# Kernel optimization log

Hardware: AMD Instinct MI355X
Metric: run time of the kernel (lower is better)

Reference implementation:

```python
import jax, jax.numpy as jnp
import numpy as np

B, T = 64, 256
CHAR_V, CHAR_D = 8000, 128
WORD_V, WORD_D = 100000, 300
POS_V, POS_D = 30, 64
SPO_D = 20
D = CHAR_D + WORD_D + POS_D + SPO_D  # 512
L, H, KD, VD, INNER = 4, 8, 64, 64, 2048
C = 25  # num tag classes


def _layer_norm(x, g, b, eps=1e-5):
    m = jnp.mean(x, axis=-1, keepdims=True)
    v = jnp.mean(jnp.square(x - m), axis=-1, keepdims=True)
    return (x - m) * jax.lax.rsqrt(v + eps) * g + b


def setup_inputs() -> dict:
    key = jax.random.key(0)
    ks = jax.random.split(key, 40)
    s = 0.05
    n = lambda k, shp, sc=0.05: jax.random.normal(k, shp, jnp.float32) * sc
    return {
        "char": jax.random.randint(ks[0], (B, T), 0, CHAR_V),
        "word": jax.random.randint(ks[1], (B, T), 0, WORD_V),
        "pos": jax.random.randint(ks[2], (B, T), 0, POS_V),
        "spo": jax.random.normal(ks[3], (B, SPO_D), jnp.float32),
        "seq_len": jax.random.randint(ks[4], (B,), 1, T + 1),
        "tag": jax.random.randint(ks[5], (B, T), 0, C),
        "char_table": n(ks[6], (CHAR_V, CHAR_D)),
        "word_table": n(ks[7], (WORD_V, WORD_D)),
        "pos_table": n(ks[8], (POS_V, POS_D)),
        "ln0_g": jnp.ones((D,), jnp.float32),
        "ln0_b": jnp.zeros((D,), jnp.float32),
        "Wq": n(ks[9], (L, D, H * KD)), "bq": jnp.zeros((L, H * KD), jnp.float32),
        "Wk": n(ks[10], (L, D, H * KD)), "bk": jnp.zeros((L, H * KD), jnp.float32),
        "Wv": n(ks[11], (L, D, H * VD)), "bv": jnp.zeros((L, H * VD), jnp.float32),
        "Wo": n(ks[12], (L, H * VD, D)), "bo": jnp.zeros((L, D), jnp.float32),
        "ln1_g": jnp.ones((L, D), jnp.float32), "ln1_b": jnp.zeros((L, D), jnp.float32),
        "W1": n(ks[13], (L, D, INNER)), "b1": jnp.zeros((L, INNER), jnp.float32),
        "W2": n(ks[14], (L, INNER, D)), "b2": jnp.zeros((L, D), jnp.float32),
        "ln2_g": jnp.ones((L, D), jnp.float32), "ln2_b": jnp.zeros((L, D), jnp.float32),
        "Wout": n(ks[15], (D, C)), "bout": jnp.zeros((C,), jnp.float32),
        "trans": n(ks[16], (C, C)),
    }


def _forward(spo, char_table, word_table, pos_table, ln0_g, ln0_b,
             Wq, bq, Wk, bk, Wv, bv, Wo, bo, ln1_g, ln1_b,
             W1, b1, W2, b2, ln2_g, ln2_b, Wout, bout, trans,
             char, word, pos, seq_len, tag):
    # mask[b,t] = t < seq_len[b]
    mask = (jnp.arange(T)[None, :] < seq_len[:, None]).astype(jnp.float32)  # [B,T]

    # embed + concat + layernorm (dropout in eval mode = identity)
    x = jnp.concatenate([
        char_table[char], word_table[word], pos_table[pos],
        jnp.broadcast_to(spo[:, None, :], (B, T, SPO_D)),
    ], axis=-1)  # [B,T,D]
    x = _layer_norm(x, ln0_g, ln0_b)

    neg_inf = jnp.finfo(x.dtype).min
    key_ok = mask[:, None, None, :] > 0  # [B,1,1,T] key padding mask
    scale = jnp.sqrt(jnp.asarray(KD, x.dtype))
    for l in range(L):
        q = (x @ Wq[l] + bq[l]).reshape(B, T, H, KD).transpose(0, 2, 1, 3)
        k = (x @ Wk[l] + bk[l]).reshape(B, T, H, KD).transpose(0, 2, 1, 3)
        v = (x @ Wv[l] + bv[l]).reshape(B, T, H, VD).transpose(0, 2, 1, 3)
        scores = jnp.einsum('bhqd,bhkd->bhqk', q, k) / scale
        scores = jnp.where(key_ok, scores, neg_inf)
        attn = jax.nn.softmax(scores, axis=-1)
        ctx = jnp.einsum('bhqk,bhkd->bhqd', attn, v).transpose(0, 2, 1, 3).reshape(B, T, H * VD)
        att_out = ctx @ Wo[l] + bo[l]
        h1 = _layer_norm(att_out + x, ln1_g[l], ln1_b[l])
        ff = jax.nn.relu(h1 @ W1[l] + b1[l]) @ W2[l] + b2[l]
        x = _layer_norm(ff + h1, ln2_g[l], ln2_b[l]) * mask[:, :, None]

    logits = x @ Wout + bout  # [B,T,C]

    # ---- CRF negative log likelihood (include_start_end_trans=False) ----
    lg = logits.transpose(1, 0, 2)  # [T,B,C]
    m = mask.T                      # [T,B]

    def step(alpha, inp):
        emit, mt = inp  # emit [B,C], mt [B]
        tmp = alpha[:, :, None] + trans[None, :, :] + emit[:, None, :]  # [B,C,C]
        new = jax.nn.logsumexp(tmp, axis=1)
        alpha = jnp.where(mt[:, None] > 0, new, alpha)
        return alpha, None

    alpha, _ = jax.lax.scan(step, lg[0], (lg[1:], m[1:]))
    log_z = jax.nn.logsumexp(alpha, axis=-1)  # [B]

    tags_t = tag.T  # [T,B]
    emit_gold = jnp.take_along_axis(lg, tags_t[:, :, None], axis=-1)[..., 0] * m  # [T,B]
    trans_gold = trans[tags_t[:-1], tags_t[1:]] * m[1:]  # [T-1,B]
    gold = emit_gold.sum(0) + trans_gold.sum(0)  # [B]

    return jnp.mean(log_z - gold)


def reference(char, word, pos, spo, seq_len, tag, char_table, word_table, pos_table,
              ln0_g, ln0_b, Wq, bq, Wk, bk, Wv, bv, Wo, bo, ln1_g, ln1_b,
              W1, b1, W2, b2, ln2_g, ln2_b, Wout, bout, trans):
    return _forward(spo, char_table, word_table, pos_table, ln0_g, ln0_b,
                    Wq, bq, Wk, bk, Wv, bv, Wo, bo, ln1_g, ln1_b,
                    W1, b1, W2, b2, ln2_g, ln2_b, Wout, bout, trans,
                    char, word, pos, seq_len, tag)
```

## Files before the change

### kernel.cpp

```cpp
#include <hip/hip_runtime.h>
#include <cmath>

namespace {

constexpr int LT = 4;
constexpr int BB = 64;
constexpr int TT = 256;
constexpr int DD = 512;
constexpr int HH = 8;
constexpr int DH = 64;
constexpr int FF = 2048;
constexpr int CC = 25;
constexpr int M_ALL = BB * TT;
constexpr size_t MB = 1024 * 1024;

typedef __attribute__((ext_vector_type(8))) short short8;
typedef __attribute__((ext_vector_type(4))) short short4_;
typedef __attribute__((ext_vector_type(4))) float f32x4;
typedef __attribute__((ext_vector_type(4))) _Float16 half4;

__device__ __forceinline__ float b2f(unsigned short u) {
  union { unsigned int i; float f; } x; x.i = ((unsigned int)u) << 16; return x.f;
}
__device__ __forceinline__ unsigned short f2b(float f) {
  union { float f; unsigned int i; } x; x.f = f;
  unsigned int r = x.i + 0x7FFFu + ((x.i >> 16) & 1u);
  return (unsigned short)(r >> 16);
}
__device__ __forceinline__ float rdlane(float v, int l) {
  union { float f; unsigned int i; } x; x.f = v;
  x.i = (unsigned int)__builtin_amdgcn_readlane((int)x.i, l);
  return x.f;
}
__device__ __forceinline__ void gl_lds16(const void* g, void* l) {
  __builtin_amdgcn_global_load_lds(
      (const __attribute__((address_space(1))) unsigned int*)g,
      (__attribute__((address_space(3))) unsigned int*)l, 16, 0, 0);
}
__device__ __forceinline__ float wredsum(float v) {
#pragma unroll
  for (int o = 32; o > 0; o >>= 1) v += __shfl_xor(v, o, 64);
  return v;
}

__global__ __launch_bounds__(64) void prefix_k(const int* __restrict__ sl,
                                               int* __restrict__ boff) {
  const int l = threadIdx.x;
  int s = sl[l];
#pragma unroll
  for (int o = 1; o < 64; o <<= 1) {
    const int u = __shfl_up(s, o, 64);
    if (l >= o) s += u;
  }
  boff[l + 1] = s;
  if (l == 0) boff[0] = 0;
}

__global__ __launch_bounds__(256) void rowmap_k(const int* __restrict__ sl,
                                                const int* __restrict__ boff,
                                                int* __restrict__ rowmap) {
  const int b = blockIdx.x, t = threadIdx.x;
  if (t < sl[b]) rowmap[boff[b] + t] = (b << 8) | t;
}

__global__ __launch_bounds__(256) void wconv_k(const float* __restrict__ in,
                                               unsigned short* __restrict__ out,
                                               int K, int N, size_t lstride) {
  __shared__ float ts[64][65];
  const int k0 = blockIdx.x * 64, n0 = blockIdx.y * 64;
  in += (size_t)blockIdx.z * K * N;
  out += (size_t)blockIdx.z * lstride;
  const int tid = threadIdx.x;
  for (int i = tid; i < 1024; i += 256) {
    const int r = i >> 4, c4 = i & 15;
    const float4 f = *(const float4*)&in[(size_t)(k0 + r) * N + n0 + c4 * 4];
    ts[r][c4 * 4 + 0] = f.x; ts[r][c4 * 4 + 1] = f.y;
    ts[r][c4 * 4 + 2] = f.z; ts[r][c4 * 4 + 3] = f.w;
  }
  __syncthreads();
  const int n_r = tid >> 2, kc = (tid & 3) * 16;
  short8 v0, v1;
#pragma unroll
  for (int j = 0; j < 8; ++j) {
    v0[j] = (short)f2b(ts[kc + j][n_r]);
    v1[j] = (short)f2b(ts[kc + 8 + j][n_r]);
  }
  unsigned short* op = out + (size_t)(n0 + n_r) * K + k0 + kc;
  *(short8*)op = v0;
  *(short8*)(op + 8) = v1;
}

__global__ __launch_bounds__(64) void embed_ln0_k(
    const int* __restrict__ ch, const int* __restrict__ wd, const int* __restrict__ ps,
    const float* __restrict__ spo, const float* __restrict__ ctab,
    const float* __restrict__ wtab, const float* __restrict__ ptab,
    const float* __restrict__ g, const float* __restrict__ be,
    const int* __restrict__ sl, const int* __restrict__ boff,
    unsigned short* __restrict__ xc) {
  const int row = blockIdx.x;
  const int b = row >> 8, t = row & 255;
  if (t >= sl[b]) return;
  const int orow = boff[b] + t;
  const int lane = threadIdx.x;
  const int ci = ch[row], wi = wd[row], pi = ps[row];
  float v[8];
#pragma unroll
  for (int j = 0; j < 2; ++j) {
    const int d = j * 256 + lane * 4;
    float4 f;
    if (d < 128)      f = *(const float4*)&ctab[(size_t)ci * 128 + d];
    else if (d < 428) f = *(const float4*)&wtab[(size_t)wi * 300 + (d - 128)];
    else if (d < 492) f = *(const float4*)&ptab[(size_t)pi * 64 + (d - 428)];
    else              f = *(const float4*)&spo[(size_t)b * 20 + (d - 492)];
    v[j * 4 + 0] = f.x; v[j * 4 + 1] = f.y; v[j * 4 + 2] = f.z; v[j * 4 + 3] = f.w;
  }
  float s = 0.f;
#pragma unroll
  for (int i = 0; i < 8; ++i) s += v[i];
  const float mean = wredsum(s) * (1.0f / 512.0f);
  float vs = 0.f;
#pragma unroll
  for (int i = 0; i < 8; ++i) { const float d = v[i] - mean; vs += d * d; }
  const float rstd = rsqrtf(wredsum(vs) * (1.0f / 512.0f) + 1e-5f);
#pragma unroll
  for (int j = 0; j < 2; ++j) {
    const int d = j * 256 + lane * 4;
    const float4 gv = *(const float4*)&g[d];
    const float4 bv = *(const float4*)&be[d];
    short4_ ob;
    ob[0] = (short)f2b((v[j * 4 + 0] - mean) * rstd * gv.x + bv.x);
    ob[1] = (short)f2b((v[j * 4 + 1] - mean) * rstd * gv.y + bv.y);
    ob[2] = (short)f2b((v[j * 4 + 2] - mean) * rstd * gv.z + bv.z);
    ob[3] = (short)f2b((v[j * 4 + 3] - mean) * rstd * gv.w + bv.w);
    *(short4_*)&xc[(size_t)orow * DD + d] = ob;
  }
}

template <int EPI>
__global__ __launch_bounds__(256) void gemm_mfma(
    const unsigned short* __restrict__ A, const unsigned short* __restrict__ Bt,
    const float* __restrict__ bias, const float* __restrict__ bias2,
    const float* __restrict__ bias3, const unsigned short* __restrict__ res,
    const int* __restrict__ Mptr, const int* __restrict__ rowmap,
    void* __restrict__ outv, void* __restrict__ out2v, void* __restrict__ out3v,
    int M, int N, int K) {
  const int Mp = Mptr[0];
  const int m0 = blockIdx.y * 128, n0 = blockIdx.x * 128;
  if (m0 >= Mp) return;
  __shared__ unsigned short As[128 * 64];
  __shared__ unsigned short Bs[128 * 64];
  const int tid = threadIdx.x;
  const int wid = tid >> 6, lane = tid & 63;
  const int wr = wid >> 1, wc = wid & 1;
  const int cl = lane & 15, rg = lane >> 4;
  f32x4 acc[4][4];
#pragma unroll
  for (int i = 0; i < 4; ++i)
#pragma unroll
    for (int j = 0; j < 4; ++j) acc[i][j] = (f32x4){0.f, 0.f, 0.f, 0.f};

  const int rbase = tid >> 3, sl = tid & 7;
  const int sc = 8 * (sl ^ (rbase & 7));

  for (int k0 = 0; k0 < K; k0 += 64) {
    if (k0) __syncthreads();
#pragma unroll
    for (int i = 0; i < 4; ++i) {
      const int r = i * 32 + rbase;
      gl_lds16(A + (size_t)(m0 + r) * K + k0 + sc, (char*)As + (i * 256 + tid) * 16);
      gl_lds16(Bt + (size_t)(n0 + r) * K + k0 + sc, (char*)Bs + (i * 256 + tid) * 16);
    }
    __syncthreads();
#pragma unroll
    for (int ks = 0; ks < 2; ++ks) {
      short8 a[4], b[4];
      const int kbyte = ks * 64 + rg * 16;
#pragma unroll
      for (int f = 0; f < 4; ++f) {
        const int am = wr * 64 + f * 16 + cl;
        a[f] = *(const short8*)((const char*)As + am * 128 + (kbyte ^ ((am & 7) << 4)));
        const int bn = wc * 64 + f * 16 + cl;
        b[f] = *(const short8*)((const char*)Bs + bn * 128 + (kbyte ^ ((bn & 7) << 4)));
      }
#pragma unroll
      for (int mi = 0; mi < 4; ++mi)
#pragma unroll
        for (int ni = 0; ni < 4; ++ni)
          acc[mi][ni] = __builtin_amdgcn_mfma_f32_16x16x32_bf16(a[mi], b[ni],
                                                                acc[mi][ni], 0, 0, 0);
    }
  }

  int rm[4][4];
  if constexpr (EPI == 5) {
#pragma unroll
    for (int mi = 0; mi < 4; ++mi) {
      const int mb_ = m0 + wr * 64 + mi * 16 + rg * 4;
#pragma unroll
      for (int i = 0; i < 4; ++i)
        rm[mi][i] = (mb_ + i < Mp) ? rowmap[mb_ + i] : -1;
    }
  }

#pragma unroll
  for (int ni = 0; ni < 4; ++ni) {
    const int n = n0 + wc * 64 + ni * 16 + cl;
    float bv;
    if constexpr (EPI == 5) {
      bv = (n < 512) ? bias[n] : (n < 1024 ? bias2[n - 512] : bias3[n - 1024]);
    } else {
      bv = bias[n];
    }
#pragma unroll
    for (int mi = 0; mi < 4; ++mi) {
      if constexpr (EPI == 5) {
        const int hh = (n >> 6) & 7, d = n & 63;
        if (n < 1024) {
          unsigned short* outp = (unsigned short*)((n < 512) ? outv : out2v);
#pragma unroll
          for (int i = 0; i < 4; ++i) {
            const int rmv = rm[mi][i];
            if (rmv >= 0) {
              const int bb = rmv >> 8, tt = rmv & 255;
              outp[(((size_t)(bb * HH + hh) * TT + tt) << 6) + d] =
                  f2b(acc[mi][ni][i] + bv);
            }
          }
        } else {
          const int rm0 = rm[mi][0];
          if (rm0 >= 0 && rm[mi][3] == rm0 + 3) {
            half4 pk;
#pragma unroll
            for (int i = 0; i < 4; ++i) pk[i] = (_Float16)(acc[mi][ni][i] + bv);
            *(half4*)((_Float16*)out3v +
                      ((((size_t)((rm0 >> 8) * HH + hh) * DH + d) << 8) + (rm0 & 255))) = pk;
          } else {
#pragma unroll
            for (int i = 0; i < 4; ++i) {
              const int rmv = rm[mi][i];
              if (rmv >= 0)
                ((_Float16*)out3v)[(((size_t)((rmv >> 8) * HH + hh) * DH + d) << 8) +
                                   (rmv & 255)] = (_Float16)(acc[mi][ni][i] + bv);
            }
          }
        }
      } else {
#pragma unroll
        for (int i = 0; i < 4; ++i) {
          const int m = m0 + wr * 64 + mi * 16 + rg * 4 + i;
          const float v = acc[mi][ni][i] + bv;
          if constexpr (EPI == 1) {
            ((unsigned short*)outv)[(size_t)m * N + n] = f2b(fmaxf(v, 0.f));
          } else if constexpr (EPI == 7) {
            ((unsigned short*)outv)[(size_t)m * N + n] =
                f2b(v + b2f(res[(size_t)m * N + n]));
          }
        }
      }
    }
  }
}

__global__ __launch_bounds__(256) void attn_mfma_k(
    const unsigned short* __restrict__ qb, const unsigned short* __restrict__ kbp,
    const _Float16* __restrict__ vtp, const int* __restrict__ seq_len,
    const int* __restrict__ boff, unsigned short* __restrict__ cb) {
  __shared__ unsigned short Ks[256 * 64];
  __shared__ _Float16 Vs[64 * 256];
  __shared__ unsigned short Os[64 * 64];
  const int bh = blockIdx.x;
  const int b = bh >> 3, h = bh & 7;
  const int tid = threadIdx.x;
  const int wid = tid >> 6, lane = tid & 63;
  const int cl = lane & 15, rg = lane >> 4;
  const int len = seq_len[b];
  const int off = boff[b];

  {
    const int r = tid >> 3, sl = tid & 7;
#pragma unroll
    for (int i = 0; i < 8; ++i) {
      if (i * 32 < len) {
        const int row = i * 32 + r;
        gl_lds16(kbp + ((size_t)bh * TT + row) * DH + 8 * (sl ^ (row & 7)),
                 (char*)Ks + (i * 256 + tid) * 16);
      }
    }
#pragma unroll
    for (int i = 0; i < 8; ++i) {
      const int u = i * 256 + tid;
      const int vrow = u >> 5, vsl = u & 31;
      gl_lds16(vtp + ((size_t)bh * DH + vrow) * TT + 8 * (vsl ^ (vrow & 7)),
               (char*)Vs + u * 16);
    }
  }
  __syncthreads();

  for (int qt4 = 0; qt4 < 4; ++qt4) {
    if (qt4 * 64 >= len) break;
    f32x4 o[4];
#pragma unroll
    for (int db = 0; db < 4; ++db) o[db] = (f32x4){0.f, 0.f, 0.f, 0.f};
    {
      const int q0 = qt4 * 64 + wid * 16;
      short8 bqf[2];
      const unsigned short* qp = qb + ((size_t)bh * TT + q0 + cl) * DH + rg * 8;
      bqf[0] = *(const short8*)qp;
      bqf[1] = *(const short8*)(qp + 32);
      f32x4 s[16];
#pragma unroll
      for (int kk = 0; kk < 16; ++kk) {
        s[kk] = (f32x4){0.f, 0.f, 0.f, 0.f};
        if (kk * 16 < len) {
          const int row = kk * 16 + cl;
          const char* base = (const char*)Ks + row * 128;
          const int sw = (row & 7) << 4;
          const short8 a0 = *(const short8*)(base + ((rg * 16) ^ sw));
          const short8 a1 = *(const short8*)(base + ((64 + rg * 16) ^ sw));
          s[kk] = __builtin_amdgcn_mfma_f32_16x16x32_bf16(a0, bqf[0], s[kk], 0, 0, 0);
          s[kk] = __builtin_amdgcn_mfma_f32_16x16x32_bf16(a1, bqf[1], s[kk], 0, 0, 0);
        }
      }
      float mx = -3.0e38f;
#pragma unroll
      for (int kk = 0; kk < 16; ++kk)
        if (kk * 16 < len) {
#pragma unroll
          for (int i = 0; i < 4; ++i) {
            float v = s[kk][i] * 0.125f;
            v = (kk * 16 + rg * 4 + i < len) ? v : -3.0e38f;
            s[kk][i] = v;
            mx = fmaxf(mx, v);
          }
        }
      mx = fmaxf(mx, __shfl_xor(mx, 16, 64));
      mx = fmaxf(mx, __shfl_xor(mx, 32, 64));
      float lsum = 0.f;
#pragma unroll
      for (int kk = 0; kk < 16; ++kk)
        if (kk * 16 < len) {
#pragma unroll
          for (int i = 0; i < 4; ++i) {
            const float p = __expf(s[kk][i] - mx);
            s[kk][i] = p;
            lsum += p;
          }
        }
      lsum += __shfl_xor(lsum, 16, 64);
      lsum += __shfl_xor(lsum, 32, 64);
      const float rl = 1.0f / lsum;
#pragma unroll
      for (int kk = 0; kk < 16; ++kk)
        if (kk * 16 < len) {
          half4 bp;
#pragma unroll
          for (int i = 0; i < 4; ++i) bp[i] = (_Float16)(s[kk][i] * rl);
#pragma unroll
          for (int db = 0; db < 4; ++db) {
            const int vrow = db * 16 + cl;
            const int byte = kk * 32 + rg * 8;
            const half4 a = *(const half4*)((const char*)Vs + vrow * 512 +
                              ((byte & ~15) ^ ((vrow & 7) << 4)) + (byte & 15));
            o[db] = __builtin_amdgcn_mfma_f32_16x16x16f16(a, bp, o[db], 0, 0, 0);
          }
        }
    }
    __syncthreads();
    {
      const int orow = wid * 16 + cl;
      char* obase = (char*)Os + orow * 128;
      const int sw = (orow & 7) << 4;
#pragma unroll
      for (int db = 0; db < 4; ++db) {
        short4_ pk;
#pragma unroll
        for (int i = 0; i < 4; ++i) pk[i] = (short)f2b(o[db][i]);
        const int byte = db * 32 + rg * 8;
        *(short4_*)(obase + ((byte & ~15) ^ sw) + (byte & 15)) = pk;
      }
    }
    __syncthreads();
    {
      const int r = tid >> 2, part = tid & 3;
      const int t = qt4 * 64 + r;
      if (t < len) {
        const int sw = (r & 7) << 4;
        const char* rbase = (const char*)Os + r * 128;
        const short8 w0 = *(const short8*)(rbase + ((part * 32) ^ sw));
        const short8 w1 = *(const short8*)(rbase + ((part * 32 + 16) ^ sw));
        unsigned short* dst = cb + ((size_t)(off + t)) * DD + h * DH + part * 16;
        *(short8*)dst = w0;
        *(short8*)(dst + 8) = w1;
      }
    }
  }
}

__global__ __launch_bounds__(64) void ln_k(const unsigned short* __restrict__ a,
                                           const float* __restrict__ g,
                                           const float* __restrict__ be,
                                           const int* __restrict__ Mptr,
                                           unsigned short* __restrict__ outb) {
  const int row = blockIdx.x;
  if (row >= Mptr[0]) return;
  const int lane = threadIdx.x;
  float v[8];
  {
    const short8 va = *(const short8*)&a[(size_t)row * DD + lane * 8];
#pragma unroll
    for (int i = 0; i < 8; ++i) v[i] = b2f((unsigned short)va[i]);
  }
  float s = 0.f;
#pragma unroll
  for (int i = 0; i < 8; ++i) s += v[i];
  const float mean = wredsum(s) * (1.0f / 512.0f);
  float vs = 0.f;
#pragma unroll
  for (int i = 0; i < 8; ++i) { const float d = v[i] - mean; vs += d * d; }
  const float rstd = rsqrtf(wredsum(vs) * (1.0f / 512.0f) + 1e-5f);
  const float4 g0 = *(const float4*)&g[lane * 8];
  const float4 g1 = *(const float4*)&g[lane * 8 + 4];
  const float4 b0 = *(const float4*)&be[lane * 8];
  const float4 b1 = *(const float4*)&be[lane * 8 + 4];
  const float gg[8] = {g0.x, g0.y, g0.z, g0.w, g1.x, g1.y, g1.z, g1.w};
  const float bb[8] = {b0.x, b0.y, b0.z, b0.w, b1.x, b1.y, b1.z, b1.w};
  short8 ob;
#pragma unroll
  for (int i = 0; i < 8; ++i)
    ob[i] = (short)f2b((v[i] - mean) * rstd * gg[i] + bb[i]);
  *(short8*)&outb[(size_t)row * DD + lane * 8] = ob;
}

__global__ __launch_bounds__(256) void logits_k(const unsigned short* __restrict__ xb,
                                                const float* __restrict__ W,
                                                const float* __restrict__ bo,
                                                const int* __restrict__ Mptr,
                                                float* __restrict__ lg) {
  const int r0 = blockIdx.x * 8;
  if (r0 >= Mptr[0]) return;
  __shared__ float xs[8][516];
  for (int i = threadIdx.x; i < 512; i += 256) {
    const int rr = i >> 6, c8 = (i & 63) * 8;
    const short8 v = *(const short8*)&xb[(size_t)(r0 + rr) * DD + c8];
#pragma unroll
    for (int j = 0; j < 8; ++j) xs[rr][c8 + j] = b2f((unsigned short)v[j]);
  }
  __syncthreads();
  const int r = threadIdx.x >> 5, c = threadIdx.x & 31;
  if (c < CC) {
    float acc = 0.f;
#pragma unroll 8
    for (int k = 0; k < DD; ++k) acc += xs[r][k] * W[k * CC + c];
    lg[(size_t)(r0 + r) * CC + c] = acc + bo[c];
  }
}

__global__ __launch_bounds__(64) void crf_k(const float* __restrict__ lg,
                                            const int* __restrict__ tag,
                                            const int* __restrict__ seq_len,
                                            const int* __restrict__ boff,
                                            const float* __restrict__ trans,
                                            float* __restrict__ nll) {
  __shared__ float eexp[TT * CC + 64];
  __shared__ float tr[CC * CC];
  const int b = blockIdx.x;
  const int l = threadIdx.x;
  const int len = seq_len[b];
  const float* lgb = lg + (size_t)boff[b] * CC;
  for (int i = l; i < len * CC; i += 64) eexp[i] = __expf(lgb[i]);
  for (int i = l; i < CC * CC; i += 64) tr[i] = trans[i];
  __syncthreads();
  const int lc = (l < CC) ? l : (CC - 1);
  float et[CC];
#pragma unroll
  for (int i = 0; i < CC; ++i) et[i] = __expf(tr[i * CC + lc]);
  const float e00 = lgb[0];
  float M = e00;
  float A = (l < CC) ? __expf(lgb[l] - e00) : 0.f;
  for (int t = 1; t < len; ++t) {
    const float e = eexp[t * CC + lc];
    float s0 = 0.f, s1 = 0.f, s2 = 0.f, s3 = 0.f, s4 = 0.f;
#pragma unroll
    for (int i = 0; i < CC; i += 5) {
      s0 += rdlane(A, i + 0) * et[i + 0];
      s1 += rdlane(A, i + 1) * et[i + 1];
      s2 += rdlane(A, i + 2) * et[i + 2];
      s3 += rdlane(A, i + 3) * et[i + 3];
      s4 += rdlane(A, i + 4) * et[i + 4];
    }
    A = (((s0 + s1) + (s2 + s3)) + s4) * e;
    if ((t & 3) == 0) {
      const float r = rdlane(A, 0);
      M += __logf(r);
      A *= __builtin_amdgcn_rcpf(r);
    }
  }
  const float tot = wredsum((l < CC) ? A : 0.f);
  float gold = 0.f;
  for (int t = l; t < len; t += 64)
    gold += lgb[t * CC + tag[b * TT + t]];
  for (int t = 1 + l; t < len; t += 64)
    gold += tr[tag[b * TT + t - 1] * CC + tag[b * TT + t]];
  gold = wredsum(gold);
  if (l == 0) nll[b] = (M + __logf(tot)) - gold;
}

__global__ __launch_bounds__(64) void final_k(const float* __restrict__ nll,
                                              float* __restrict__ out) {
  float v = nll[threadIdx.x];
  v = wredsum(v);
  if (threadIdx.x == 0) out[0] = v * (1.0f / 64.0f);
}

}

extern "C" void kernel_launch(void* const* d_in, const int* in_sizes, int n_in,
                              void* d_out, int out_size, void* d_ws, size_t ws_size,
                              hipStream_t stream) {
  (void)in_sizes; (void)n_in; (void)out_size; (void)ws_size;
  const int* chi = (const int*)d_in[0];
  const int* wdi = (const int*)d_in[1];
  const int* psi = (const int*)d_in[2];
  const float* spo = (const float*)d_in[3];
  const int* seq_len = (const int*)d_in[4];
  const int* tag = (const int*)d_in[5];
  const float* ctab = (const float*)d_in[6];
  const float* wtab = (const float*)d_in[7];
  const float* ptab = (const float*)d_in[8];
  const float* ln0g = (const float*)d_in[9];
  const float* ln0b = (const float*)d_in[10];
  const float* Wq = (const float*)d_in[11];
  const float* bq = (const float*)d_in[12];
  const float* Wk = (const float*)d_in[13];
  const float* bk = (const float*)d_in[14];
  const float* Wv = (const float*)d_in[15];
  const float* bv = (const float*)d_in[16];
  const float* Wo = (const float*)d_in[17];
  const float* bo = (const float*)d_in[18];
  const float* ln1g = (const float*)d_in[19];
  const float* ln1b = (const float*)d_in[20];
  const float* W1 = (const float*)d_in[21];
  const float* b1 = (const float*)d_in[22];
  const float* W2 = (const float*)d_in[23];
  const float* b2 = (const float*)d_in[24];
  const float* ln2g = (const float*)d_in[25];
  const float* ln2b = (const float*)d_in[26];
  const float* Wout = (const float*)d_in[27];
  const float* bout = (const float*)d_in[28];
  const float* trans = (const float*)d_in[29];

  char* w8 = (char*)d_ws;
  unsigned short* ib  = (unsigned short*)(w8);
  unsigned short* xc  = (unsigned short*)(w8 + 64 * MB);
  unsigned short* cbx = (unsigned short*)(w8 + 80 * MB);
  unsigned short* ab  = (unsigned short*)(w8 + 96 * MB);
  unsigned short* hb  = (unsigned short*)(w8 + 112 * MB);
  unsigned short* t0b = (unsigned short*)(w8 + 128 * MB);
  unsigned short* qbuf = (unsigned short*)(w8 + 144 * MB);
  unsigned short* kbuf = (unsigned short*)(w8 + 160 * MB);
  _Float16* vtb = (_Float16*)(w8 + 176 * MB);
  unsigned short* wqkv = (unsigned short*)(w8 + 192 * MB);
  unsigned short* wot = (unsigned short*)(w8 + 198 * MB);
  unsigned short* w1t = (unsigned short*)(w8 + 200 * MB);
  unsigned short* w2t = (unsigned short*)(w8 + 208 * MB);
  float* lg = (float*)(w8 + 216 * MB);
  float* nll = (float*)(w8 + 218 * MB);
  int* boff = (int*)(w8 + 219 * MB);
  int* rowmap = (int*)(w8 + 220 * MB);
  const int* Mptr = boff + 64;

  prefix_k<<<1, 64, 0, stream>>>(seq_len, boff);
  rowmap_k<<<BB, 256, 0, stream>>>(seq_len, boff, rowmap);

  const size_t QKVS = (size_t)1536 * 512;
  wconv_k<<<dim3(8, 8, LT), 256, 0, stream>>>(Wq, wqkv, DD, DD, QKVS);
  wconv_k<<<dim3(8, 8, LT), 256, 0, stream>>>(Wk, wqkv + 512 * 512, DD, DD, QKVS);
  wconv_k<<<dim3(8, 8, LT), 256, 0, stream>>>(Wv, wqkv + 1024 * 512, DD, DD, QKVS);
  wconv_k<<<dim3(8, 8, LT), 256, 0, stream>>>(Wo, wot, DD, DD, (size_t)DD * DD);
  wconv_k<<<dim3(8, 32, LT), 256, 0, stream>>>(W1, w1t, DD, FF, (size_t)DD * FF);
  wconv_k<<<dim3(32, 8, LT), 256, 0, stream>>>(W2, w2t, FF, DD, (size_t)FF * DD);

  embed_ln0_k<<<M_ALL, 64, 0, stream>>>(chi, wdi, psi, spo, ctab, wtab, ptab,
                                        ln0g, ln0b, seq_len, boff, xc);

  for (int l = 0; l < LT; ++l) {
    gemm_mfma<5><<<dim3(12, 128), 256, 0, stream>>>(
        xc, wqkv + (size_t)l * QKVS, bq + l * DD, bk + l * DD, bv + l * DD,
        nullptr, Mptr, rowmap, qbuf, kbuf, vtb, M_ALL, 1536, DD);
    attn_mfma_k<<<BB * HH, 256, 0, stream>>>(qbuf, kbuf, vtb, seq_len, boff, cbx);
    gemm_mfma<7><<<dim3(4, 128), 256, 0, stream>>>(
        cbx, wot + (size_t)l * DD * DD, bo + l * DD, nullptr, nullptr,
        xc, Mptr, nullptr, ab, nullptr, nullptr, M_ALL, DD, DD);
    ln_k<<<M_ALL, 64, 0, stream>>>(ab, ln1g + l * DD, ln1b + l * DD, Mptr, hb);
    gemm_mfma<1><<<dim3(FF / 128, 128), 256, 0, stream>>>(
        hb, w1t + (size_t)l * FF * DD, b1 + l * FF, nullptr, nullptr,
        nullptr, Mptr, nullptr, ib, nullptr, nullptr, M_ALL, FF, DD);
    gemm_mfma<7><<<dim3(DD / 128, 128), 256, 0, stream>>>(
        ib, w2t + (size_t)l * FF * DD, b2 + l * DD, nullptr, nullptr,
        hb, Mptr, nullptr, t0b, nullptr, nullptr, M_ALL, DD, FF);
    ln_k<<<M_ALL, 64, 0, stream>>>(t0b, ln2g + l * DD, ln2b + l * DD, Mptr, xc);
  }
  logits_k<<<M_ALL / 8, 256, 0, stream>>>(xc, Wout, bout, Mptr, lg);
  crf_k<<<BB, 64, 0, stream>>>(lg, tag, seq_len, boff, trans, nll);
  final_k<<<1, 64, 0, stream>>>(nll, (float*)d_out);
}
```

Baseline: 821.3 us.

## Double-buffer GEMM LDS tiles and pack four rows per block in LN kernels

The MFMA GEMM now keeps two LDS buffers for the A and B tiles and issues the global-to-LDS loads for the next k-tile before computing on the current one. This is meant to overlap memory latency with MFMA work, at the cost of doubling LDS use to 64KB per block, which may reduce occupancy. It relies on a single barrier per iteration to order the asynchronous LDS writes, which may not fully wait on the direct-to-LDS loads. Separately, the embedding+LN0 and LayerNorm kernels now process four rows per 256-thread block instead of one row per 64-thread block, cutting the number of blocks launched.

```diff
diff --git a/kernel.cpp b/kernel.cpp
--- a/kernel.cpp
+++ b/kernel.cpp
@@ -90,18 +90,18 @@
   *(short8*)(op + 8) = v1;
 }
 
-__global__ __launch_bounds__(64) void embed_ln0_k(
+__global__ __launch_bounds__(256) void embed_ln0_k(
     const int* __restrict__ ch, const int* __restrict__ wd, const int* __restrict__ ps,
     const float* __restrict__ spo, const float* __restrict__ ctab,
     const float* __restrict__ wtab, const float* __restrict__ ptab,
     const float* __restrict__ g, const float* __restrict__ be,
     const int* __restrict__ sl, const int* __restrict__ boff,
     unsigned short* __restrict__ xc) {
-  const int row = blockIdx.x;
+  const int row = blockIdx.x * 4 + (threadIdx.x >> 6);
   const int b = row >> 8, t = row & 255;
   if (t >= sl[b]) return;
   const int orow = boff[b] + t;
-  const int lane = threadIdx.x;
+  const int lane = threadIdx.x & 63;
   const int ci = ch[row], wi = wd[row], pi = ps[row];
   float v[8];
 #pragma unroll
@@ -147,8 +147,8 @@
   const int Mp = Mptr[0];
   const int m0 = blockIdx.y * 128, n0 = blockIdx.x * 128;
   if (m0 >= Mp) return;
-  __shared__ unsigned short As[128 * 64];
-  __shared__ unsigned short Bs[128 * 64];
+  __shared__ unsigned short As[2][128 * 64];
+  __shared__ unsigned short Bs[2][128 * 64];
   const int tid = threadIdx.x;
   const int wid = tid >> 6, lane = tid & 63;
   const int wr = wid >> 1, wc = wid & 1;
@@ -162,15 +162,22 @@
   const int rbase = tid >> 3, sl = tid & 7;
   const int sc = 8 * (sl ^ (rbase & 7));
 
-  for (int k0 = 0; k0 < K; k0 += 64) {
-    if (k0) __syncthreads();
+  auto stage = [&](int buf, int k0) {
 #pragma unroll
     for (int i = 0; i < 4; ++i) {
       const int r = i * 32 + rbase;
-      gl_lds16(A + (size_t)(m0 + r) * K + k0 + sc, (char*)As + (i * 256 + tid) * 16);
-      gl_lds16(Bt + (size_t)(n0 + r) * K + k0 + sc, (char*)Bs + (i * 256 + tid) * 16);
-    }
-    __syncthreads();
+      gl_lds16(A + (size_t)(m0 + r) * K + k0 + sc,
+               (char*)As[buf] + (i * 256 + tid) * 16);
+      gl_lds16(Bt + (size_t)(n0 + r) * K + k0 + sc,
+               (char*)Bs[buf] + (i * 256 + tid) * 16);
+    }
+  };
+
+  stage(0, 0);
+  __syncthreads();
+  int cur = 0;
+  for (int k0 = 0; k0 < K; k0 += 64) {
+    if (k0 + 64 < K) stage(cur ^ 1, k0 + 64);
 #pragma unroll
     for (int ks = 0; ks < 2; ++ks) {
       short8 a[4], b[4];
@@ -178,9 +185,11 @@
 #pragma unroll
       for (int f = 0; f < 4; ++f) {
         const int am = wr * 64 + f * 16 + cl;
-        a[f] = *(const short8*)((const char*)As + am * 128 + (kbyte ^ ((am & 7) << 4)));
+        a[f] = *(const short8*)((const char*)As[cur] + am * 128 +
+                                (kbyte ^ ((am & 7) << 4)));
         const int bn = wc * 64 + f * 16 + cl;
-        b[f] = *(const short8*)((const char*)Bs + bn * 128 + (kbyte ^ ((bn & 7) << 4)));
+        b[f] = *(const short8*)((const char*)Bs[cur] + bn * 128 +
+                                (kbyte ^ ((bn & 7) << 4)));
       }
 #pragma unroll
       for (int mi = 0; mi < 4; ++mi)
@@ -189,6 +198,8 @@
           acc[mi][ni] = __builtin_amdgcn_mfma_f32_16x16x32_bf16(a[mi], b[ni],
                                                                 acc[mi][ni], 0, 0, 0);
     }
+    __syncthreads();
+    cur ^= 1;
   }
 
   int rm[4][4];
@@ -396,14 +407,14 @@
   }
 }
 
-__global__ __launch_bounds__(64) void ln_k(const unsigned short* __restrict__ a,
-                                           const float* __restrict__ g,
-                                           const float* __restrict__ be,
-                                           const int* __restrict__ Mptr,
-                                           unsigned short* __restrict__ outb) {
-  const int row = blockIdx.x;
+__global__ __launch_bounds__(256) void ln_k(const unsigned short* __restrict__ a,
+                                            const float* __restrict__ g,
+                                            const float* __restrict__ be,
+                                            const int* __restrict__ Mptr,
+                                            unsigned short* __restrict__ outb) {
+  const int row = blockIdx.x * 4 + (threadIdx.x >> 6);
   if (row >= Mptr[0]) return;
-  const int lane = threadIdx.x;
+  const int lane = threadIdx.x & 63;
   float v[8];
   {
     const short8 va = *(const short8*)&a[(size_t)row * DD + lane * 8];
@@ -580,8 +591,8 @@
   wconv_k<<<dim3(8, 32, LT), 256, 0, stream>>>(W1, w1t, DD, FF, (size_t)DD * FF);
   wconv_k<<<dim3(32, 8, LT), 256, 0, stream>>>(W2, w2t, FF, DD, (size_t)FF * DD);
 
-  embed_ln0_k<<<M_ALL, 64, 0, stream>>>(chi, wdi, psi, spo, ctab, wtab, ptab,
-                                        ln0g, ln0b, seq_len, boff, xc);
+  embed_ln0_k<<<M_ALL / 4, 256, 0, stream>>>(chi, wdi, psi, spo, ctab, wtab, ptab,
+                                             ln0g, ln0b, seq_len, boff, xc);
 
   for (int l = 0; l < LT; ++l) {
     gemm_mfma<5><<<dim3(12, 128), 256, 0, stream>>>(
@@ -591,14 +602,14 @@
     gemm_mfma<7><<<dim3(4, 128), 256, 0, stream>>>(
         cbx, wot + (size_t)l * DD * DD, bo + l * DD, nullptr, nullptr,
         xc, Mptr, nullptr, ab, nullptr, nullptr, M_ALL, DD, DD);
-    ln_k<<<M_ALL, 64, 0, stream>>>(ab, ln1g + l * DD, ln1b + l * DD, Mptr, hb);
+    ln_k<<<M_ALL / 4, 256, 0, stream>>>(ab, ln1g + l * DD, ln1b + l * DD, Mptr, hb);
     gemm_mfma<1><<<dim3(FF / 128, 128), 256, 0, stream>>>(
         hb, w1t + (size_t)l * FF * DD, b1 + l * FF, nullptr, nullptr,
         nullptr, Mptr, nullptr, ib, nullptr, nullptr, M_ALL, FF, DD);
     gemm_mfma<7><<<dim3(DD / 128, 128), 256, 0, stream>>>(
         ib, w2t + (size_t)l * FF * DD, b2 + l * DD, nullptr, nullptr,
         hb, Mptr, nullptr, t0b, nullptr, nullptr, M_ALL, DD, FF);
-    ln_k<<<M_ALL, 64, 0, stream>>>(t0b, ln2g + l * DD, ln2b + l * DD, Mptr, xc);
+    ln_k<<<M_ALL / 4, 256, 0, stream>>>(t0b, ln2g + l * DD, ln2b + l * DD, Mptr, xc);
   }
   logits_k<<<M_ALL / 8, 256, 0, stream>>>(xc, Wout, bout, Mptr, lg);
   crf_k<<<BB, 64, 0, stream>>>(lg, tag, seq_len, boff, trans, nll);
```

Result: no change. 814.8 us (-0.8%).
